# Performance work log

Hardware: AMD Instinct MI355X
Metric: run time of the kernel (lower is better)

## Reference

```python
import jax, jax.numpy as jnp
import numpy as np

ALPHA = 0.2   # LeakyReLU negative slope
T_STEPS = 10  # diffusion iterations


def setup_inputs() -> dict:
    key = jax.random.key(0)
    ks = jax.random.split(key, 7)
    N, F, H, C, E, NTRAIN = 8192, 512, 64, 10, 262144, 512
    # glorot-ish scales so exp(leaky_relu(.)) stays in range
    h = jax.random.normal(ks[0], (N, F), jnp.float32)
    W = jax.random.normal(ks[1], (H, F), jnp.float32) * 0.059
    a = jax.random.normal(ks[2], (2 * H, 1), jnp.float32) * 0.12
    W1 = jax.random.normal(ks[3], (C, F), jnp.float32) * 0.06
    features = jax.random.normal(ks[4], (N, F), jnp.float32)
    edge_index = jax.random.randint(ks[5], (2, E), 0, N, dtype=jnp.int32)
    idx_train = jnp.arange(NTRAIN, dtype=jnp.int32)
    labels = jax.random.randint(ks[6], (N,), 0, C, dtype=jnp.int32)
    return {"h": h, "W": W, "a": a, "W1": W1, "features": features,
            "edge_index": edge_index, "idx_train": idx_train, "labels": labels}


def reference(h, W, a, W1, features, edge_index, idx_train, labels):
    N = h.shape[0]
    C = W1.shape[0]
    # ---- CalAttenA ----
    Wh = h @ W.T                                   # [N, H]
    src, dst = edge_index[0], edge_index[1]
    f12 = jnp.concatenate([Wh[src], Wh[dst]], axis=1)   # [E, 2H]
    e = jnp.exp(jax.nn.leaky_relu(f12 @ a, negative_slope=ALPHA)).ravel()  # [E]
    A = jnp.zeros((N, N), Wh.dtype).at[src, dst].set(e)
    s1 = A.sum(axis=1)
    diag = jnp.arange(N)
    A = A.at[diag, diag].add(jnp.where(s1 == 0, 1.0, 0.0).astype(Wh.dtype))
    A = A / A.sum(axis=1, keepdims=True)           # row-normalized attention
    # ---- PoiConv ----
    Kg = jnp.zeros((C, N), Wh.dtype).at[labels[idx_train], idx_train].set(1.0)
    c = Kg.sum(axis=1) / idx_train.shape[0]        # [C]
    b = Kg.T.at[idx_train].add(-c)                 # [N, C] (idx_train unique)
    # D = diag(1 / rowsum(A + 1e-10*I)); eye only touches the diagonal so
    # rowsum is rowsum(A) + 1e-10 == 1 + 1e-10 after normalization.
    d = 1.0 / (A.sum(axis=1) + 1e-10)              # [N]
    P = d[:, None] * A.T                           # D @ A^T
    Db = d[:, None] * b                            # D @ b
    ut = jnp.zeros((N, C), Wh.dtype)
    for t in range(1, T_STEPS + 1):
        ut = P @ ut + Db
        if t == T_STEPS - 3:  # isadj == False branch; dropout inactive (eval)
            ut = ut + features @ W1.T
    return ut
```

## Files before the change

kernel.cpp:

```cpp
#include <hip/hip_runtime.h>
#include <stdint.h>

#define NN 8192
#define FF 512
#define HH 64
#define CC 10
#define PAD 12
#define EE 262144
#define NTR 512
#define ALPHA_NS 0.2f

#define CAP 96u
#define EMPTY 0xFFFFFFFFu
#define ROWS_PB 32
#define SLOTS_PB ((NN*CAP)/256u)

__device__ __forceinline__ float dot4(float4 a, float4 b){
    return a.x*b.x + a.y*b.y + a.z*b.z + a.w*b.w;
}

__global__ __launch_bounds__(1024) void k_init(
    const float* __restrict__ W, const float* __restrict__ a,
    const float* __restrict__ h, const float* __restrict__ feat,
    const float* __restrict__ W1, const int* __restrict__ idx_tr,
    const int* __restrict__ labels,
    uint32_t* __restrict__ csrc2, float* __restrict__ s1,
    float* __restrict__ s_src, float* __restrict__ s_dst,
    float* __restrict__ FW, float* __restrict__ Db)
{
    __shared__ float v0l[FF];
    __shared__ float v1l[FF];
    __shared__ int chist[CC];
    __shared__ float cvecl[CC];
    __shared__ uint8_t lmark[ROWS_PB];

    const int tid = threadIdx.x;
    const int b   = blockIdx.x;
    const int rbase = b * ROWS_PB;

    for (uint32_t i = tid; i < SLOTS_PB; i += 1024)
        csrc2[(uint32_t)b*SLOTS_PB + i] = EMPTY;
    if (tid < ROWS_PB) s1[rbase + tid] = 0.f;

    {
        int f = tid & (FF-1);
        const float* av = (tid < FF) ? a : (a + HH);
        float acc = 0.f;
        for (int hh = 0; hh < HH; ++hh) acc += W[hh*FF + f] * av[hh];
        if (tid < FF) v0l[f] = acc; else v1l[f] = acc;
    }

    if (tid < ROWS_PB) lmark[tid] = 0;
    if (tid < CC) chist[tid] = 0;
    __syncthreads();
    if (tid < NTR){
        int node = idx_tr[tid];
        atomicAdd(&chist[labels[node]], 1);
        unsigned lr = (unsigned)(node - rbase);
        if (lr < (unsigned)ROWS_PB) lmark[lr] = 1;
    }
    __syncthreads();
    if (tid < CC) cvecl[tid] = (float)chist[tid] / (float)NTR;
    __syncthreads();

    {
        const int wid = tid >> 6, lane = tid & 63;
        const float4* v0 = (const float4*)v0l;
        const float4* v1 = (const float4*)v1l;
        #pragma unroll
        for (int rr = 0; rr < 2; ++rr){
            int row = rbase + wid*2 + rr;
            const float4* hr = (const float4*)(h + (size_t)row*FF);
            float4 x0 = hr[lane*2], x1 = hr[lane*2+1];
            float a0 = dot4(x0, v0[lane*2]) + dot4(x1, v0[lane*2+1]);
            float a1 = dot4(x0, v1[lane*2]) + dot4(x1, v1[lane*2+1]);
            #pragma unroll
            for (int off = 32; off >= 1; off >>= 1){
                a0 += __shfl_xor(a0, off);
                a1 += __shfl_xor(a1, off);
            }
            if (lane == 0){ s_src[row] = a0; s_dst[row] = a1; }

            const float4* fr = (const float4*)(feat + (size_t)row*FF);
            float4 f0 = fr[lane*2], f1 = fr[lane*2+1];
            float acc[CC];
            #pragma unroll
            for (int c = 0; c < CC; ++c){
                const float4* wr = (const float4*)(W1 + c*FF);
                acc[c] = dot4(f0, wr[lane*2]) + dot4(f1, wr[lane*2+1]);
            }
            #pragma unroll
            for (int c = 0; c < CC; ++c){
                float r = acc[c];
                #pragma unroll
                for (int off = 32; off >= 1; off >>= 1) r += __shfl_xor(r, off);
                acc[c] = r;
            }
            if (lane == 0){
                #pragma unroll
                for (int c = 0; c < CC; ++c) FW[row*PAD + c] = acc[c];
            }
        }
    }

    if (tid < ROWS_PB*PAD){
        int il = tid / PAD, c = tid - il*PAD;
        int row = rbase + il;
        float v = 0.f;
        if (c < CC && lmark[il]) v = ((labels[row] == c) ? 1.0f : 0.0f) - cvecl[c];
        Db[row*PAD + c] = v;
    }
}

__global__ void k_build(const int* __restrict__ ei, const float* __restrict__ s_src,
                        const float* __restrict__ s_dst,
                        uint32_t* __restrict__ csrc2, float* __restrict__ e2,
                        float* __restrict__ s1)
{
    int k = blockIdx.x*256 + threadIdx.x;
    int src = ei[k], dst = ei[EE + k];
    uint32_t base = (uint32_t)dst * CAP;
    uint32_t p = (uint32_t)(((uint64_t)((uint32_t)src * 2654435761u) * CAP) >> 32);
    float z = s_src[src] + s_dst[dst];
    z = (z >= 0.f) ? z : ALPHA_NS * z;
    float e = expf(z);
    for (uint32_t it = 0; it < CAP; ++it){
        uint32_t prev = atomicCAS(&csrc2[base + p], EMPTY, (uint32_t)src);
        if (prev == EMPTY){
            e2[base + p] = e;
            atomicAdd(&s1[src], e);
            break;
        }
        if (prev == (uint32_t)src) break;
        p = (p + 1u == CAP) ? 0u : p + 1u;
    }
}

__global__ __launch_bounds__(1024) void k_fixup(
    const uint32_t* __restrict__ csrc2, const float* __restrict__ e2,
    const float* __restrict__ s1, uint2* __restrict__ tabc,
    uint32_t* __restrict__ cnt)
{
    const int tid = threadIdx.x;
    const int wid = tid >> 6, lane = tid & 63;
    const int row = blockIdx.x*16 + wid;
    const uint32_t base = (uint32_t)row * CAP;

    uint32_t c0 = csrc2[base + lane];
    uint32_t c1 = (lane < (int)(CAP - 64u)) ? csrc2[base + 64 + lane] : EMPTY;
    float    e0 = e2[base + lane];
    float    e1 = (lane < (int)(CAP - 64u)) ? e2[base + 64 + lane] : 0.f;

    uint64_t m0 = __ballot(c0 != EMPTY);
    uint64_t m1 = __ballot((lane < (int)(CAP - 64u)) && c1 != EMPTY);
    uint64_t below = (1ull << lane) - 1ull;
    uint32_t t0   = (uint32_t)__popcll(m0);
    uint32_t pos0 = (uint32_t)__popcll(m0 & below);
    uint32_t pos1 = t0 + (uint32_t)__popcll(m1 & below);
    uint32_t total = t0 + (uint32_t)__popcll(m1);

    if (c0 != EMPTY){
        float w = e0 / s1[c0];
        tabc[base + pos0] = make_uint2(c0, __float_as_uint(w));
    }
    if (lane < (int)(CAP - 64u) && c1 != EMPTY){
        float w = e1 / s1[c1];
        tabc[base + pos1] = make_uint2(c1, __float_as_uint(w));
    }

    if (lane == 0){
        if (s1[row] == 0.f){
            tabc[base + total] = make_uint2((uint32_t)row, __float_as_uint(1.0f));
            total += 1u;
        }
        cnt[row] = total;
    }
}

__global__ __launch_bounds__(256) void k_spmv(
    const uint32_t* __restrict__ cnt, const uint2* __restrict__ tabc,
    const float* __restrict__ uh_in, const float* __restrict__ Db,
    const float* __restrict__ FW, float* __restrict__ uout,
    int add_fw, int final_step)
{
    const int tid = threadIdx.x;
    const int wid = tid >> 6, lane = tid & 63;
    const int l16 = lane & 15;
    const int row = blockIdx.x*16 + wid*4 + (lane >> 4);
    const uint2* tp = tabc + (uint32_t)row * CAP;
    const uint32_t n = cnt[row];

    float acc[PAD];
    #pragma unroll
    for (int c = 0; c < PAD; ++c) acc[c] = 0.f;
    for (uint32_t p = (uint32_t)l16; p < n; p += 16u){
        uint2 v = tp[p];
        float w = __uint_as_float(v.y);
        const float4* u4 = (const float4*)(uh_in + (size_t)v.x*PAD);
        float4 u0 = u4[0], u1 = u4[1], u2 = u4[2];
        acc[0] += w*u0.x; acc[1] += w*u0.y; acc[2]  += w*u0.z; acc[3]  += w*u0.w;
        acc[4] += w*u1.x; acc[5] += w*u1.y; acc[6]  += w*u1.z; acc[7]  += w*u1.w;
        acc[8] += w*u2.x; acc[9] += w*u2.y; acc[10] += w*u2.z; acc[11] += w*u2.w;
    }
    #pragma unroll
    for (int c = 0; c < PAD; ++c){
        float r = acc[c];
        #pragma unroll
        for (int off = 8; off >= 1; off >>= 1) r += __shfl_xor(r, off, 16);
        acc[c] = r;
    }
    float v = acc[0];
    #pragma unroll
    for (int c = 1; c < PAD; ++c) v = (l16 == c) ? acc[c] : v;
    if (l16 < CC){
        v += Db[row*PAD + l16];
        if (add_fw) v += FW[row*PAD + l16];
    } else {
        v = 0.f;
    }
    if (final_step){
        if (l16 < CC) uout[(size_t)row*CC + l16] = v;
    } else {
        if (l16 < PAD) uout[(size_t)row*PAD + l16] = v;
    }
}

extern "C" void kernel_launch(void* const* d_in, const int* in_sizes, int n_in,
                              void* d_out, int out_size, void* d_ws, size_t ws_size,
                              hipStream_t stream){
    const float* h    = (const float*)d_in[0];
    const float* W    = (const float*)d_in[1];
    const float* a    = (const float*)d_in[2];
    const float* W1   = (const float*)d_in[3];
    const float* feat = (const float*)d_in[4];
    const int* ei     = (const int*)d_in[5];
    const int* idx_tr = (const int*)d_in[6];
    const int* labels = (const int*)d_in[7];
    float* out = (float*)d_out;

    char* wsp = (char*)d_ws;
    auto alloc = [&](size_t bytes)->void*{
        void* p = (void*)wsp;
        wsp += (bytes + 255) & ~(size_t)255;
        return p;
    };
    uint32_t* csrc2 = (uint32_t*)alloc((size_t)NN*CAP*4);
    float*    e2    = (float*)   alloc((size_t)NN*CAP*4);
    uint2*    tabc  = (uint2*)   alloc((size_t)NN*CAP*8);
    float*    s1    = (float*)   alloc(NN*4);
    uint32_t* cnt   = (uint32_t*)alloc(NN*4);
    float*    s_src = (float*)   alloc(NN*4);
    float*    s_dst = (float*)   alloc(NN*4);
    float*    FW    = (float*)   alloc((size_t)NN*PAD*4);
    float*    Db    = (float*)   alloc((size_t)NN*PAD*4);
    float*    uA    = (float*)   alloc((size_t)NN*PAD*4);
    float*    uB    = (float*)   alloc((size_t)NN*PAD*4);

    k_init <<<256, 1024, 0, stream>>>(W, a, h, feat, W1, idx_tr, labels,
                                      csrc2, s1, s_src, s_dst, FW, Db);
    k_build<<<EE/256, 256, 0, stream>>>(ei, s_src, s_dst, csrc2, e2, s1);
    k_fixup<<<NN/16, 1024, 0, stream>>>(csrc2, e2, s1, tabc, cnt);

    const float* cur = Db;
    for (int t = 2; t <= 10; ++t){
        float* dst = (t == 10) ? out : ((t & 1) ? uB : uA);
        k_spmv<<<NN/16, 256, 0, stream>>>(cnt, tabc, cur, Db, FW, dst,
                                          (t == 7) ? 1 : 0, (t == 10) ? 1 : 0);
        cur = dst;
    }
}
```

Before: 103.0 us.

## Move attention weight computation to fixup and fold row normalization into SpMV output

The build kernel now only inserts source keys into the per-destination hash table, with no exp, no e2 store and no global atomicAdd on s1. The fixup kernel compacts each table and computes the edge weights there, accumulating row sums in per-block shared memory. A new reduction kernel combines those partial sums, handles empty rows and prescales Db. The division by s1 is no longer stored per edge; it becomes a per-row scale on the SpMV output, which removes the global atomic contention and the extra e2 pass at the cost of a 128x8192 partial-sum buffer and one more launch.

```diff
diff --git a/kernel.cpp b/kernel.cpp
--- a/kernel.cpp
+++ b/kernel.cpp
@@ -14,6 +14,7 @@
 #define EMPTY 0xFFFFFFFFu
 #define ROWS_PB 32
 #define SLOTS_PB ((NN*CAP)/256u)
+#define FB 128
 
 __device__ __forceinline__ float dot4(float4 a, float4 b){
     return a.x*b.x + a.y*b.y + a.z*b.z + a.w*b.w;
@@ -24,7 +25,7 @@
     const float* __restrict__ h, const float* __restrict__ feat,
     const float* __restrict__ W1, const int* __restrict__ idx_tr,
     const int* __restrict__ labels,
-    uint32_t* __restrict__ csrc2, float* __restrict__ s1,
+    uint32_t* __restrict__ csrc2,
     float* __restrict__ s_src, float* __restrict__ s_dst,
     float* __restrict__ FW, float* __restrict__ Db)
 {
@@ -40,7 +41,6 @@
 
     for (uint32_t i = tid; i < SLOTS_PB; i += 1024)
         csrc2[(uint32_t)b*SLOTS_PB + i] = EMPTY;
-    if (tid < ROWS_PB) s1[rbase + tid] = 0.f;
 
     {
         int f = tid & (FF-1);
@@ -112,76 +112,90 @@
     }
 }
 
-__global__ void k_build(const int* __restrict__ ei, const float* __restrict__ s_src,
-                        const float* __restrict__ s_dst,
-                        uint32_t* __restrict__ csrc2, float* __restrict__ e2,
-                        float* __restrict__ s1)
+__global__ void k_build(const int* __restrict__ ei, uint32_t* __restrict__ csrc2)
 {
     int k = blockIdx.x*256 + threadIdx.x;
-    int src = ei[k], dst = ei[EE + k];
-    uint32_t base = (uint32_t)dst * CAP;
-    uint32_t p = (uint32_t)(((uint64_t)((uint32_t)src * 2654435761u) * CAP) >> 32);
-    float z = s_src[src] + s_dst[dst];
-    z = (z >= 0.f) ? z : ALPHA_NS * z;
-    float e = expf(z);
+    uint32_t src = (uint32_t)ei[k];
+    uint32_t dst = (uint32_t)ei[EE + k];
+    uint32_t base = dst * CAP;
+    uint32_t p = (uint32_t)(((uint64_t)(src * 2654435761u) * CAP) >> 32);
     for (uint32_t it = 0; it < CAP; ++it){
-        uint32_t prev = atomicCAS(&csrc2[base + p], EMPTY, (uint32_t)src);
-        if (prev == EMPTY){
-            e2[base + p] = e;
-            atomicAdd(&s1[src], e);
-            break;
+        uint32_t prev = atomicCAS(&csrc2[base + p], EMPTY, src);
+        if (prev == EMPTY || prev == src) break;
+        p = (p + 1u == CAP) ? 0u : p + 1u;
+    }
+}
+
+__global__ __launch_bounds__(1024) void k_fixup(
+    const uint32_t* __restrict__ csrc2, const float* __restrict__ s_src,
+    const float* __restrict__ s_dst, uint2* __restrict__ tabc,
+    uint32_t* __restrict__ cnt, float* __restrict__ s1p)
+{
+    __shared__ float s1l[NN];
+    const int tid = threadIdx.x;
+    const int b   = blockIdx.x;
+    const int wid = tid >> 6, lane = tid & 63;
+    const int g   = lane >> 4, l16 = lane & 15;
+    const int row = (b*16 + wid)*4 + g;
+    const uint32_t base = (uint32_t)row * CAP;
+
+    for (int i = tid; i < NN; i += 1024) s1l[i] = 0.f;
+    __syncthreads();
+
+    const float sdst = s_dst[row];
+    uint32_t running = 0;
+    #pragma unroll
+    for (int step = 0; step < 6; ++step){
+        uint32_t key = csrc2[base + step*16 + l16];
+        bool valid = (key != EMPTY);
+        uint64_t bal = __ballot(valid);
+        uint32_t grp = (uint32_t)((bal >> (g*16)) & 0xFFFFull);
+        uint32_t rank = (uint32_t)__popc(grp & ((1u << l16) - 1u));
+        if (valid){
+            float z = s_src[key] + sdst;
+            z = (z >= 0.f) ? z : ALPHA_NS * z;
+            float e = expf(z);
+            tabc[base + running + rank] = make_uint2(key, __float_as_uint(e));
+            atomicAdd(&s1l[key], e);
         }
-        if (prev == (uint32_t)src) break;
-        p = (p + 1u == CAP) ? 0u : p + 1u;
-    }
-}
-
-__global__ __launch_bounds__(1024) void k_fixup(
-    const uint32_t* __restrict__ csrc2, const float* __restrict__ e2,
-    const float* __restrict__ s1, uint2* __restrict__ tabc,
-    uint32_t* __restrict__ cnt)
-{
-    const int tid = threadIdx.x;
-    const int wid = tid >> 6, lane = tid & 63;
-    const int row = blockIdx.x*16 + wid;
-    const uint32_t base = (uint32_t)row * CAP;
-
-    uint32_t c0 = csrc2[base + lane];
-    uint32_t c1 = (lane < (int)(CAP - 64u)) ? csrc2[base + 64 + lane] : EMPTY;
-    float    e0 = e2[base + lane];
-    float    e1 = (lane < (int)(CAP - 64u)) ? e2[base + 64 + lane] : 0.f;
-
-    uint64_t m0 = __ballot(c0 != EMPTY);
-    uint64_t m1 = __ballot((lane < (int)(CAP - 64u)) && c1 != EMPTY);
-    uint64_t below = (1ull << lane) - 1ull;
-    uint32_t t0   = (uint32_t)__popcll(m0);
-    uint32_t pos0 = (uint32_t)__popcll(m0 & below);
-    uint32_t pos1 = t0 + (uint32_t)__popcll(m1 & below);
-    uint32_t total = t0 + (uint32_t)__popcll(m1);
-
-    if (c0 != EMPTY){
-        float w = e0 / s1[c0];
-        tabc[base + pos0] = make_uint2(c0, __float_as_uint(w));
-    }
-    if (lane < (int)(CAP - 64u) && c1 != EMPTY){
-        float w = e1 / s1[c1];
-        tabc[base + pos1] = make_uint2(c1, __float_as_uint(w));
-    }
-
-    if (lane == 0){
-        if (s1[row] == 0.f){
-            tabc[base + total] = make_uint2((uint32_t)row, __float_as_uint(1.0f));
-            total += 1u;
-        }
-        cnt[row] = total;
+        running += (uint32_t)__popc(grp);
+    }
+    if (l16 == 0) cnt[row] = running;
+    __syncthreads();
+    for (int i = tid; i < NN; i += 1024) s1p[(size_t)b*NN + i] = s1l[i];
+}
+
+__global__ __launch_bounds__(256) void k_s1red(
+    const float* __restrict__ s1p, uint2* __restrict__ tabc,
+    uint32_t* __restrict__ cnt, const float* __restrict__ Db,
+    float* __restrict__ invs1, float* __restrict__ uh1)
+{
+    int row = blockIdx.x*256 + threadIdx.x;
+    float s = 0.f;
+    for (int b = 0; b < FB; ++b) s += s1p[(size_t)b*NN + row];
+    if (s == 0.f){
+        uint32_t c = cnt[row];
+        tabc[(uint32_t)row*CAP + c] = make_uint2((uint32_t)row, __float_as_uint(1.0f));
+        cnt[row] = c + 1u;
+        s = 1.0f;
+    }
+    float inv = 1.0f / s;
+    invs1[row] = inv;
+    const float4* d4 = (const float4*)(Db + (size_t)row*PAD);
+    float4* u4 = (float4*)(uh1 + (size_t)row*PAD);
+    #pragma unroll
+    for (int q = 0; q < 3; ++q){
+        float4 v = d4[q];
+        v.x *= inv; v.y *= inv; v.z *= inv; v.w *= inv;
+        u4[q] = v;
     }
 }
 
 __global__ __launch_bounds__(256) void k_spmv(
     const uint32_t* __restrict__ cnt, const uint2* __restrict__ tabc,
     const float* __restrict__ uh_in, const float* __restrict__ Db,
-    const float* __restrict__ FW, float* __restrict__ uout,
-    int add_fw, int final_step)
+    const float* __restrict__ FW, const float* __restrict__ invs1,
+    float* __restrict__ uout, int add_fw, int final_step)
 {
     const int tid = threadIdx.x;
     const int wid = tid >> 6, lane = tid & 63;
@@ -221,6 +235,7 @@
     if (final_step){
         if (l16 < CC) uout[(size_t)row*CC + l16] = v;
     } else {
+        v *= invs1[row];
         if (l16 < PAD) uout[(size_t)row*PAD + l16] = v;
     }
 }
@@ -245,10 +260,10 @@
         return p;
     };
     uint32_t* csrc2 = (uint32_t*)alloc((size_t)NN*CAP*4);
-    float*    e2    = (float*)   alloc((size_t)NN*CAP*4);
     uint2*    tabc  = (uint2*)   alloc((size_t)NN*CAP*8);
-    float*    s1    = (float*)   alloc(NN*4);
+    float*    s1p   = (float*)   alloc((size_t)FB*NN*4);
     uint32_t* cnt   = (uint32_t*)alloc(NN*4);
+    float*    invs1 = (float*)   alloc(NN*4);
     float*    s_src = (float*)   alloc(NN*4);
     float*    s_dst = (float*)   alloc(NN*4);
     float*    FW    = (float*)   alloc((size_t)NN*PAD*4);
@@ -257,14 +272,15 @@
     float*    uB    = (float*)   alloc((size_t)NN*PAD*4);
 
     k_init <<<256, 1024, 0, stream>>>(W, a, h, feat, W1, idx_tr, labels,
-                                      csrc2, s1, s_src, s_dst, FW, Db);
-    k_build<<<EE/256, 256, 0, stream>>>(ei, s_src, s_dst, csrc2, e2, s1);
-    k_fixup<<<NN/16, 1024, 0, stream>>>(csrc2, e2, s1, tabc, cnt);
-
-    const float* cur = Db;
+                                      csrc2, s_src, s_dst, FW, Db);
+    k_build<<<EE/256, 256, 0, stream>>>(ei, csrc2);
+    k_fixup<<<FB, 1024, 0, stream>>>(csrc2, s_src, s_dst, tabc, cnt, s1p);
+    k_s1red<<<NN/256, 256, 0, stream>>>(s1p, tabc, cnt, Db, invs1, uA);
+
+    const float* cur = uA;
     for (int t = 2; t <= 10; ++t){
-        float* dst = (t == 10) ? out : ((t & 1) ? uB : uA);
-        k_spmv<<<NN/16, 256, 0, stream>>>(cnt, tabc, cur, Db, FW, dst,
+        float* dst = (t == 10) ? out : ((t & 1) ? uA : uB);
+        k_spmv<<<NN/16, 256, 0, stream>>>(cnt, tabc, cur, Db, FW, invs1, dst,
                                           (t == 7) ? 1 : 0, (t == 10) ? 1 : 0);
         cur = dst;
     }
```

Measured after the change: 99.40 us. -3.5%, faster.
